# Optimization experiments

Measured on AMD Instinct MI355X. Metric: run time of the kernel, lower is better.

## Reference

```python
import jax, jax.numpy as jnp
import numpy as np

BETA = 0.9      # membrane decay
THRESH = 1.0    # firing threshold


def _lif(x):
    """Leaky integrate-and-fire over leading time axis. x: (T, ..., C) -> spikes (T, ..., C)."""
    def step(mem, xt):
        mem = BETA * mem + xt
        s = (mem > THRESH).astype(xt.dtype)
        mem = mem - s * THRESH  # soft reset
        return mem, s
    _, spikes = jax.lax.scan(step, jnp.zeros_like(x[0]), x)
    return spikes


def setup_inputs() -> dict:
    key = jax.random.key(0)
    k1, k2, k3, k4, k5 = jax.random.split(key, 5)
    T, N, D = 4, 8192, 1024
    E, EF, TOPK = 8, 512, 2  # expert_ff = d_ff // n_experts = 4096 // 8
    x = jax.random.normal(k1, (T, N, D), dtype=jnp.float32)
    expert_indices = jax.random.randint(k2, (N, TOPK), 0, E)
    expert_weights = jax.random.uniform(k3, (N, TOPK), dtype=jnp.float32)
    up_w = jax.random.normal(k4, (E, EF, D), dtype=jnp.float32) * 0.02   # Linear(d_model, ef).weight
    down_w = jax.random.normal(k5, (E, D, EF), dtype=jnp.float32) * 0.02  # Linear(ef, d_model).weight
    return {"x": x, "expert_indices": expert_indices, "expert_weights": expert_weights,
            "up_w": up_w, "down_w": down_w}


def reference(x, expert_indices, expert_weights, up_w, down_w):
    T, N, D = x.shape
    E = up_w.shape[0]
    # Dense combine weights W[n, e] = sum_k weights[n, k] * (indices[n, k] == e)
    W = jnp.zeros((N, E), dtype=x.dtype).at[
        jnp.arange(N)[:, None], expert_indices].add(expert_weights)
    out = jnp.zeros_like(x)
    for e in range(E):  # fixed small loop over experts
        h = _lif(jnp.einsum('tnd,fd->tnf', x, up_w[e]))   # up-proj + LIF hidden
        o = _lif(jnp.einsum('tnf,df->tnd', h, down_w[e]))  # down-proj + LIF output
        out = out + o * W[:, e][None, :, None]             # weighted combine (0 for inactive)
    return out
```

## Files before the change

kernel.cpp:

```cpp
#include <hip/hip_runtime.h>
#include <stdint.h>

#define T_STEPS 4
#define NTOK    8192
#define DMODEL  1024
#define NEXP    8
#define EFF     512
#define BMT     128
#define CAPTOT  (2*NTOK + NEXP*BMT)

typedef __attribute__((ext_vector_type(8))) short bf8_t;
typedef __attribute__((ext_vector_type(4))) float f32x4;

#define MFMA(a,b,c) __builtin_amdgcn_mfma_f32_16x16x32_bf16((a),(b),(c),0,0,0)


__device__ __forceinline__ unsigned short bf16rn(float f) {
    unsigned u = __float_as_uint(f);
    unsigned r = u + 0x7fffu + ((u >> 16) & 1u);
    return (unsigned short)(r >> 16);
}
__device__ __forceinline__ float bf2f(unsigned short h) {
    return __uint_as_float(((unsigned)h) << 16);
}
__device__ __forceinline__ unsigned pk(unsigned short a, unsigned short b) {
    return (unsigned)a | ((unsigned)b << 16);
}

__device__ __forceinline__ void stage8_3limb(const float* __restrict__ src,
                                             unsigned short* d0, unsigned short* d1,
                                             unsigned short* d2) {
    float v[8];
    *(float4*)&v[0] = *(const float4*)(src + 0);
    *(float4*)&v[4] = *(const float4*)(src + 4);
    unsigned short h[8], m[8], l[8];
#pragma unroll
    for (int i = 0; i < 8; ++i) {
        unsigned short a = bf16rn(v[i]);
        float r1 = v[i] - bf2f(a);
        unsigned short b = bf16rn(r1);
        float r2 = r1 - bf2f(b);
        h[i] = a; m[i] = b; l[i] = bf16rn(r2);
    }
    *(uint4*)d0 = make_uint4(pk(h[0],h[1]), pk(h[2],h[3]), pk(h[4],h[5]), pk(h[6],h[7]));
    *(uint4*)d1 = make_uint4(pk(m[0],m[1]), pk(m[2],m[3]), pk(m[4],m[5]), pk(m[6],m[7]));
    *(uint4*)d2 = make_uint4(pk(l[0],l[1]), pk(l[2],l[3]), pk(l[4],l[5]), pk(l[6],l[7]));
}


__global__ void k_split(const float* __restrict__ w, unsigned short* __restrict__ h,
                        unsigned short* __restrict__ m, unsigned short* __restrict__ l) {
    size_t i = (size_t)(blockIdx.x * blockDim.x + threadIdx.x) * 8;
    stage8_3limb(w + i, h + i, m + i, l + i);
}


__global__ void k_count(const int* __restrict__ idx, int* __restrict__ counts) {
    int n = blockIdx.x * blockDim.x + threadIdx.x;
    if (n >= NTOK) return;
    int e0 = idx[2*n], e1 = idx[2*n+1];
    atomicAdd(&counts[e0], 1);
    if (e1 != e0) atomicAdd(&counts[e1], 1);
}

__global__ void k_prefix(const int* __restrict__ counts, int* __restrict__ offsets) {
    if (threadIdx.x == 0) {
        int o = 0;
        for (int e = 0; e < NEXP; ++e) {
            offsets[e] = o;
            o += (counts[e] + BMT - 1) / BMT * BMT;
        }
        offsets[NEXP] = o;
    }
}

__global__ void k_fill(const int* __restrict__ idx, const float* __restrict__ wts,
                       const int* __restrict__ offsets, int* __restrict__ cursors,
                       int* __restrict__ tok, float* __restrict__ wgt) {
    int n = blockIdx.x * blockDim.x + threadIdx.x;
    if (n >= NTOK) return;
    int e0 = idx[2*n], e1 = idx[2*n+1];
    float w0 = wts[2*n], w1 = wts[2*n+1];
    if (e0 == e1) w0 = __fadd_rn(w0, w1);
    int p0 = offsets[e0] + atomicAdd(&cursors[e0], 1);
    tok[p0] = n; wgt[p0] = w0;
    if (e1 != e0) {
        int p1 = offsets[e1] + atomicAdd(&cursors[e1], 1);
        tok[p1] = n; wgt[p1] = w1;
    }
}


__global__ __launch_bounds__(256, 2)
void k_up(const float* __restrict__ x,
          const unsigned short* __restrict__ uwh, const unsigned short* __restrict__ uwm,
          const unsigned short* __restrict__ uwl,
          const int* __restrict__ offsets, const int* __restrict__ tok,
          unsigned short* __restrict__ spk) {
    const int m0 = blockIdx.x * BMT;
    const int ft = blockIdx.y;
    if (m0 >= offsets[NEXP]) return;
    int e = 0;
    for (int i = 1; i < NEXP; ++i) if (m0 >= offsets[i]) e = i;

    __shared__ unsigned short As[3][128][40];
    __shared__ unsigned short Bs[3][128][40];

    const int tid  = threadIdx.x;
    const int lane = tid & 63, wid = tid >> 6;
    const int quad = lane >> 4, l16 = lane & 15;
    const int mw = (wid & 1) * 64, nw = (wid >> 1) * 64;

    const int r = tid >> 1, half = tid & 1;
    const int tokA = tok[m0 + r];
    const float* xbase = x + (size_t)tokA * DMODEL + half * 16;
    const size_t woff = ((size_t)e * EFF + ft * 128 + r) * DMODEL + half * 16;
    const unsigned short* bhp = uwh + woff;
    const unsigned short* bmp = uwm + woff;
    const unsigned short* blp = uwl + woff;

    f32x4 mem[4][4];
#pragma unroll
    for (int i = 0; i < 4; ++i)
#pragma unroll
        for (int j = 0; j < 4; ++j) mem[i][j] = (f32x4){0.f,0.f,0.f,0.f};

    for (int t = 0; t < T_STEPS; ++t) {
        f32x4 acc[4][4];
#pragma unroll
        for (int i = 0; i < 4; ++i)
#pragma unroll
            for (int j = 0; j < 4; ++j) acc[i][j] = (f32x4){0.f,0.f,0.f,0.f};

        const float* xrow = xbase + (size_t)t * NTOK * DMODEL;

        for (int kc = 0; kc < DMODEL; kc += 32) {
            __syncthreads();
            stage8_3limb(xrow + kc,     &As[0][r][half*16],   &As[1][r][half*16],   &As[2][r][half*16]);
            stage8_3limb(xrow + kc + 8, &As[0][r][half*16+8], &As[1][r][half*16+8], &As[2][r][half*16+8]);
            *(uint4*)&Bs[0][r][half*16]   = *(const uint4*)(bhp + kc);
            *(uint4*)&Bs[0][r][half*16+8] = *(const uint4*)(bhp + kc + 8);
            *(uint4*)&Bs[1][r][half*16]   = *(const uint4*)(bmp + kc);
            *(uint4*)&Bs[1][r][half*16+8] = *(const uint4*)(bmp + kc + 8);
            *(uint4*)&Bs[2][r][half*16]   = *(const uint4*)(blp + kc);
            *(uint4*)&Bs[2][r][half*16+8] = *(const uint4*)(blp + kc + 8);
            __syncthreads();

            bf8_t bh[4], bm[4], bl[4];
#pragma unroll
            for (int nt = 0; nt < 4; ++nt) {
                const int nr = nw + nt*16 + l16;
                bh[nt] = *(const bf8_t*)&Bs[0][nr][quad*8];
                bm[nt] = *(const bf8_t*)&Bs[1][nr][quad*8];
                bl[nt] = *(const bf8_t*)&Bs[2][nr][quad*8];
            }
#pragma unroll
            for (int mt = 0; mt < 4; ++mt) {
                const int mr = mw + mt*16 + l16;
                bf8_t ah = *(const bf8_t*)&As[0][mr][quad*8];
                bf8_t am = *(const bf8_t*)&As[1][mr][quad*8];
                bf8_t al = *(const bf8_t*)&As[2][mr][quad*8];
#pragma unroll
                for (int nt = 0; nt < 4; ++nt) {
                    f32x4 c = acc[mt][nt];
                    c = MFMA(ah, bh[nt], c);
                    c = MFMA(am, bh[nt], c);
                    c = MFMA(ah, bm[nt], c);
                    c = MFMA(am, bm[nt], c);
                    c = MFMA(al, bh[nt], c);
                    c = MFMA(ah, bl[nt], c);
                    acc[mt][nt] = c;
                }
            }
        }

#pragma unroll
        for (int mt = 0; mt < 4; ++mt)
#pragma unroll
            for (int nt = 0; nt < 4; ++nt)
#pragma unroll
                for (int reg = 0; reg < 4; ++reg) {
                    float mv = __fadd_rn(__fmul_rn(0.9f, mem[mt][nt][reg]), acc[mt][nt][reg]);
                    bool s = mv > 1.0f;
                    mem[mt][nt][reg] = __fsub_rn(mv, s ? 1.0f : 0.0f);
                    int row = m0 + mw + mt*16 + quad*4 + reg;
                    int col = ft*128 + nw + nt*16 + l16;
                    spk[((size_t)t * CAPTOT + row) * EFF + col] = s ? 0x3F80u : 0u;
                }
    }
}


__global__ __launch_bounds__(256, 3)
void k_dn(const unsigned short* __restrict__ spk,
          const unsigned short* __restrict__ dwh, const unsigned short* __restrict__ dwm,
          const unsigned short* __restrict__ dwl,
          const int* __restrict__ offsets, const int* __restrict__ tok,
          const float* __restrict__ wgt, float* __restrict__ out) {
    const int m0 = blockIdx.x * BMT;
    const int dt = blockIdx.y;
    if (m0 >= offsets[NEXP]) return;
    int e = 0;
    for (int i = 1; i < NEXP; ++i) if (m0 >= offsets[i]) e = i;

    __shared__ unsigned short As[128][40];
    __shared__ unsigned short Bs[3][64][40];

    const int tid  = threadIdx.x;
    const int lane = tid & 63, wid = tid >> 6;
    const int quad = lane >> 4, l16 = lane & 15;
    const int mw = (wid & 1) * 64, nw = (wid >> 1) * 32;

    const int r = tid >> 1, half = tid & 1;
    const int dr = tid >> 2, q = tid & 3;
    const unsigned short* arow = spk + (size_t)(m0 + r) * EFF + half * 16;
    const size_t doff = ((size_t)e * DMODEL + dt * 64 + dr) * EFF + q * 8;
    const unsigned short* bhp = dwh + doff;
    const unsigned short* bmp = dwm + doff;
    const unsigned short* blp = dwl + doff;

    int   rn[4][4];
    float rw[4][4];
#pragma unroll
    for (int mt = 0; mt < 4; ++mt)
#pragma unroll
        for (int reg = 0; reg < 4; ++reg) {
            int rr = m0 + mw + mt*16 + quad*4 + reg;
            rn[mt][reg] = tok[rr];
            rw[mt][reg] = wgt[rr];
        }

    f32x4 mem[4][2];
#pragma unroll
    for (int i = 0; i < 4; ++i) { mem[i][0] = (f32x4){0.f,0.f,0.f,0.f}; mem[i][1] = (f32x4){0.f,0.f,0.f,0.f}; }

    for (int t = 0; t < T_STEPS; ++t) {
        f32x4 acc[4][2];
#pragma unroll
        for (int i = 0; i < 4; ++i) { acc[i][0] = (f32x4){0.f,0.f,0.f,0.f}; acc[i][1] = (f32x4){0.f,0.f,0.f,0.f}; }

        const unsigned short* at = arow + (size_t)t * CAPTOT * EFF;

        for (int kc = 0; kc < EFF; kc += 32) {
            __syncthreads();
            *(uint4*)&As[r][half*16 + 0] = *(const uint4*)(at + kc + 0);
            *(uint4*)&As[r][half*16 + 8] = *(const uint4*)(at + kc + 8);
            *(uint4*)&Bs[0][dr][q*8] = *(const uint4*)(bhp + kc);
            *(uint4*)&Bs[1][dr][q*8] = *(const uint4*)(bmp + kc);
            *(uint4*)&Bs[2][dr][q*8] = *(const uint4*)(blp + kc);
            __syncthreads();

            bf8_t bh[2], bm[2], bl[2];
#pragma unroll
            for (int nt = 0; nt < 2; ++nt) {
                const int nr = nw + nt*16 + l16;
                bh[nt] = *(const bf8_t*)&Bs[0][nr][quad*8];
                bm[nt] = *(const bf8_t*)&Bs[1][nr][quad*8];
                bl[nt] = *(const bf8_t*)&Bs[2][nr][quad*8];
            }
#pragma unroll
            for (int mt = 0; mt < 4; ++mt) {
                const int mr = mw + mt*16 + l16;
                bf8_t a = *(const bf8_t*)&As[mr][quad*8];
#pragma unroll
                for (int nt = 0; nt < 2; ++nt) {
                    f32x4 c = acc[mt][nt];
                    c = MFMA(a, bh[nt], c);
                    c = MFMA(a, bm[nt], c);
                    c = MFMA(a, bl[nt], c);
                    acc[mt][nt] = c;
                }
            }
        }

#pragma unroll
        for (int mt = 0; mt < 4; ++mt)
#pragma unroll
            for (int nt = 0; nt < 2; ++nt)
#pragma unroll
                for (int reg = 0; reg < 4; ++reg) {
                    float mv = __fadd_rn(__fmul_rn(0.9f, mem[mt][nt][reg]), acc[mt][nt][reg]);
                    bool s = mv > 1.0f;
                    mem[mt][nt][reg] = __fsub_rn(mv, s ? 1.0f : 0.0f);
                    float w = rw[mt][reg];
                    if (s && w != 0.0f) {
                        int col = dt*64 + nw + nt*16 + l16;
                        atomicAdd(out + ((size_t)t * NTOK + rn[mt][reg]) * DMODEL + col, w);
                    }
                }
    }
}


extern "C" void kernel_launch(void* const* d_in, const int* in_sizes, int n_in,
                              void* d_out, int out_size, void* d_ws, size_t ws_size,
                              hipStream_t stream) {
    const float* x      = (const float*)d_in[0];
    const int*   idx    = (const int*)  d_in[1];
    const float* wts    = (const float*)d_in[2];
    const float* up_w   = (const float*)d_in[3];
    const float* down_w = (const float*)d_in[4];
    float* out = (float*)d_out;

    char* ws = (char*)d_ws;
    int*   counts  = (int*)(ws + 0);
    int*   cursors = (int*)(ws + 32);
    int*   offsets = (int*)(ws + 64);
    int*   tok     = (int*)(ws + 128);
    float* wgt     = (float*)(ws + 128 + (size_t)CAPTOT * 4);
    unsigned short* spk = (unsigned short*)(ws + 128 + (size_t)CAPTOT * 8);

    const size_t WSPK = (size_t)T_STEPS * CAPTOT * EFF * 2;
    size_t base2 = 128 + (size_t)CAPTOT * 8 + WSPK;
    base2 = (base2 + 511) & ~(size_t)511;
    const size_t WLIMB = (size_t)NEXP * EFF * DMODEL * 2;
    unsigned short* uwh = (unsigned short*)(ws + base2);
    unsigned short* uwm = (unsigned short*)(ws + base2 + 1*WLIMB);
    unsigned short* uwl = (unsigned short*)(ws + base2 + 2*WLIMB);
    unsigned short* dwh = (unsigned short*)(ws + base2 + 3*WLIMB);
    unsigned short* dwm = (unsigned short*)(ws + base2 + 4*WLIMB);
    unsigned short* dwl = (unsigned short*)(ws + base2 + 5*WLIMB);

    hipMemsetAsync(ws, 0, 128 + (size_t)CAPTOT * 8, stream);
    hipMemsetAsync(out, 0, (size_t)out_size * sizeof(float), stream);

    const int nsplit = NEXP * EFF * DMODEL / 8 / 256;
    k_split<<<nsplit, 256, 0, stream>>>(up_w,   uwh, uwm, uwl);
    k_split<<<nsplit, 256, 0, stream>>>(down_w, dwh, dwm, dwl);

    k_count <<<(NTOK + 255) / 256, 256, 0, stream>>>(idx, counts);
    k_prefix<<<1, 64, 0, stream>>>(counts, offsets);
    k_fill  <<<(NTOK + 255) / 256, 256, 0, stream>>>(idx, wts, offsets, cursors, tok, wgt);

    dim3 gup(CAPTOT / BMT, EFF / 128);
    k_up<<<gup, 256, 0, stream>>>(x, uwh, uwm, uwl, offsets, tok, spk);

    dim3 gdn(CAPTOT / BMT, DMODEL / 64);
    k_dn<<<gdn, 256, 0, stream>>>(spk, dwh, dwm, dwl, offsets, tok, wgt, out);
}
```

Baseline: 1.071 ms.

## Swizzle LDS tiles, widen down-proj tile to 128 columns, raise k_up occupancy

Replaces the padded LDS rows (stride 40) with unpadded 32-wide rows that use an XOR column swizzle, which shrinks shared memory and is meant to avoid bank conflicts. k_up's launch bound rises to 3 blocks per CU, since the smaller LDS footprint allows it. k_dn now computes a 128x128 output tile per block instead of 128x64, halving the grid in the D dimension and the number of times each spike tile is reloaded. Token and weight lookups move into the epilogue to save registers. The larger accumulator set in k_dn raises register pressure and may reduce its occupancy.

```diff
diff --git a/kernel.cpp b/kernel.cpp
--- a/kernel.cpp
+++ b/kernel.cpp
@@ -13,6 +13,8 @@
 typedef __attribute__((ext_vector_type(4))) float f32x4;
 
 #define MFMA(a,b,c) __builtin_amdgcn_mfma_f32_16x16x32_bf16((a),(b),(c),0,0,0)
+
+#define SWZC(r, c) ((((c) ^ (((r) >> 1) & 3))) * 8)
 
 
 __device__ __forceinline__ unsigned short bf16rn(float f) {
@@ -91,7 +93,7 @@
 }
 
 
-__global__ __launch_bounds__(256, 2)
+__global__ __launch_bounds__(256, 3)
 void k_up(const float* __restrict__ x,
           const unsigned short* __restrict__ uwh, const unsigned short* __restrict__ uwm,
           const unsigned short* __restrict__ uwl,
@@ -103,8 +105,8 @@
     int e = 0;
     for (int i = 1; i < NEXP; ++i) if (m0 >= offsets[i]) e = i;
 
-    __shared__ unsigned short As[3][128][40];
-    __shared__ unsigned short Bs[3][128][40];
+    __shared__ unsigned short As[3][128][32];
+    __shared__ unsigned short Bs[3][128][32];
 
     const int tid  = threadIdx.x;
     const int lane = tid & 63, wid = tid >> 6;
@@ -112,6 +114,8 @@
     const int mw = (wid & 1) * 64, nw = (wid >> 1) * 64;
 
     const int r = tid >> 1, half = tid & 1;
+    const int c0 = SWZC(r, half*2 + 0);
+    const int c1 = SWZC(r, half*2 + 1);
     const int tokA = tok[m0 + r];
     const float* xbase = x + (size_t)tokA * DMODEL + half * 16;
     const size_t woff = ((size_t)e * EFF + ft * 128 + r) * DMODEL + half * 16;
@@ -119,6 +123,8 @@
     const unsigned short* bmp = uwm + woff;
     const unsigned short* blp = uwl + woff;
 
+    const int kq = SWZC(l16, quad);
+
     f32x4 mem[4][4];
 #pragma unroll
     for (int i = 0; i < 4; ++i)
@@ -136,30 +142,30 @@
 
         for (int kc = 0; kc < DMODEL; kc += 32) {
             __syncthreads();
-            stage8_3limb(xrow + kc,     &As[0][r][half*16],   &As[1][r][half*16],   &As[2][r][half*16]);
-            stage8_3limb(xrow + kc + 8, &As[0][r][half*16+8], &As[1][r][half*16+8], &As[2][r][half*16+8]);
-            *(uint4*)&Bs[0][r][half*16]   = *(const uint4*)(bhp + kc);
-            *(uint4*)&Bs[0][r][half*16+8] = *(const uint4*)(bhp + kc + 8);
-            *(uint4*)&Bs[1][r][half*16]   = *(const uint4*)(bmp + kc);
-            *(uint4*)&Bs[1][r][half*16+8] = *(const uint4*)(bmp + kc + 8);
-            *(uint4*)&Bs[2][r][half*16]   = *(const uint4*)(blp + kc);
-            *(uint4*)&Bs[2][r][half*16+8] = *(const uint4*)(blp + kc + 8);
+            stage8_3limb(xrow + kc,     &As[0][r][c0], &As[1][r][c0], &As[2][r][c0]);
+            stage8_3limb(xrow + kc + 8, &As[0][r][c1], &As[1][r][c1], &As[2][r][c1]);
+            *(uint4*)&Bs[0][r][c0] = *(const uint4*)(bhp + kc);
+            *(uint4*)&Bs[0][r][c1] = *(const uint4*)(bhp + kc + 8);
+            *(uint4*)&Bs[1][r][c0] = *(const uint4*)(bmp + kc);
+            *(uint4*)&Bs[1][r][c1] = *(const uint4*)(bmp + kc + 8);
+            *(uint4*)&Bs[2][r][c0] = *(const uint4*)(blp + kc);
+            *(uint4*)&Bs[2][r][c1] = *(const uint4*)(blp + kc + 8);
             __syncthreads();
 
             bf8_t bh[4], bm[4], bl[4];
 #pragma unroll
             for (int nt = 0; nt < 4; ++nt) {
                 const int nr = nw + nt*16 + l16;
-                bh[nt] = *(const bf8_t*)&Bs[0][nr][quad*8];
-                bm[nt] = *(const bf8_t*)&Bs[1][nr][quad*8];
-                bl[nt] = *(const bf8_t*)&Bs[2][nr][quad*8];
+                bh[nt] = *(const bf8_t*)&Bs[0][nr][kq];
+                bm[nt] = *(const bf8_t*)&Bs[1][nr][kq];
+                bl[nt] = *(const bf8_t*)&Bs[2][nr][kq];
             }
 #pragma unroll
             for (int mt = 0; mt < 4; ++mt) {
                 const int mr = mw + mt*16 + l16;
-                bf8_t ah = *(const bf8_t*)&As[0][mr][quad*8];
-                bf8_t am = *(const bf8_t*)&As[1][mr][quad*8];
-                bf8_t al = *(const bf8_t*)&As[2][mr][quad*8];
+                bf8_t ah = *(const bf8_t*)&As[0][mr][kq];
+                bf8_t am = *(const bf8_t*)&As[1][mr][kq];
+                bf8_t al = *(const bf8_t*)&As[2][mr][kq];
 #pragma unroll
                 for (int nt = 0; nt < 4; ++nt) {
                     f32x4 c = acc[mt][nt];
@@ -203,67 +209,66 @@
     int e = 0;
     for (int i = 1; i < NEXP; ++i) if (m0 >= offsets[i]) e = i;
 
-    __shared__ unsigned short As[128][40];
-    __shared__ unsigned short Bs[3][64][40];
+    __shared__ unsigned short As[128][32];
+    __shared__ unsigned short Bs[3][128][32];
 
     const int tid  = threadIdx.x;
     const int lane = tid & 63, wid = tid >> 6;
     const int quad = lane >> 4, l16 = lane & 15;
-    const int mw = (wid & 1) * 64, nw = (wid >> 1) * 32;
+    const int mw = (wid & 1) * 64, nw = (wid >> 1) * 64;
 
     const int r = tid >> 1, half = tid & 1;
-    const int dr = tid >> 2, q = tid & 3;
+    const int c0 = SWZC(r, half*2 + 0);
+    const int c1 = SWZC(r, half*2 + 1);
     const unsigned short* arow = spk + (size_t)(m0 + r) * EFF + half * 16;
-    const size_t doff = ((size_t)e * DMODEL + dt * 64 + dr) * EFF + q * 8;
+    const size_t doff = ((size_t)e * DMODEL + dt * 128 + r) * EFF + half * 16;
     const unsigned short* bhp = dwh + doff;
     const unsigned short* bmp = dwm + doff;
     const unsigned short* blp = dwl + doff;
 
-    int   rn[4][4];
-    float rw[4][4];
-#pragma unroll
-    for (int mt = 0; mt < 4; ++mt)
-#pragma unroll
-        for (int reg = 0; reg < 4; ++reg) {
-            int rr = m0 + mw + mt*16 + quad*4 + reg;
-            rn[mt][reg] = tok[rr];
-            rw[mt][reg] = wgt[rr];
-        }
-
-    f32x4 mem[4][2];
-#pragma unroll
-    for (int i = 0; i < 4; ++i) { mem[i][0] = (f32x4){0.f,0.f,0.f,0.f}; mem[i][1] = (f32x4){0.f,0.f,0.f,0.f}; }
+    const int kq = SWZC(l16, quad);
+
+    f32x4 mem[4][4];
+#pragma unroll
+    for (int i = 0; i < 4; ++i)
+#pragma unroll
+        for (int j = 0; j < 4; ++j) mem[i][j] = (f32x4){0.f,0.f,0.f,0.f};
 
     for (int t = 0; t < T_STEPS; ++t) {
-        f32x4 acc[4][2];
-#pragma unroll
-        for (int i = 0; i < 4; ++i) { acc[i][0] = (f32x4){0.f,0.f,0.f,0.f}; acc[i][1] = (f32x4){0.f,0.f,0.f,0.f}; }
+        f32x4 acc[4][4];
+#pragma unroll
+        for (int i = 0; i < 4; ++i)
+#pragma unroll
+            for (int j = 0; j < 4; ++j) acc[i][j] = (f32x4){0.f,0.f,0.f,0.f};
 
         const unsigned short* at = arow + (size_t)t * CAPTOT * EFF;
 
         for (int kc = 0; kc < EFF; kc += 32) {
             __syncthreads();
-            *(uint4*)&As[r][half*16 + 0] = *(const uint4*)(at + kc + 0);
-            *(uint4*)&As[r][half*16 + 8] = *(const uint4*)(at + kc + 8);
-            *(uint4*)&Bs[0][dr][q*8] = *(const uint4*)(bhp + kc);
-            *(uint4*)&Bs[1][dr][q*8] = *(const uint4*)(bmp + kc);
-            *(uint4*)&Bs[2][dr][q*8] = *(const uint4*)(blp + kc);
+            *(uint4*)&As[r][c0] = *(const uint4*)(at + kc + 0);
+            *(uint4*)&As[r][c1] = *(const uint4*)(at + kc + 8);
+            *(uint4*)&Bs[0][r][c0] = *(const uint4*)(bhp + kc);
+            *(uint4*)&Bs[0][r][c1] = *(const uint4*)(bhp + kc + 8);
+            *(uint4*)&Bs[1][r][c0] = *(const uint4*)(bmp + kc);
+            *(uint4*)&Bs[1][r][c1] = *(const uint4*)(bmp + kc + 8);
+            *(uint4*)&Bs[2][r][c0] = *(const uint4*)(blp + kc);
+            *(uint4*)&Bs[2][r][c1] = *(const uint4*)(blp + kc + 8);
             __syncthreads();
 
-            bf8_t bh[2], bm[2], bl[2];
-#pragma unroll
-            for (int nt = 0; nt < 2; ++nt) {
+            bf8_t bh[4], bm[4], bl[4];
+#pragma unroll
+            for (int nt = 0; nt < 4; ++nt) {
                 const int nr = nw + nt*16 + l16;
-                bh[nt] = *(const bf8_t*)&Bs[0][nr][quad*8];
-                bm[nt] = *(const bf8_t*)&Bs[1][nr][quad*8];
-                bl[nt] = *(const bf8_t*)&Bs[2][nr][quad*8];
+                bh[nt] = *(const bf8_t*)&Bs[0][nr][kq];
+                bm[nt] = *(const bf8_t*)&Bs[1][nr][kq];
+                bl[nt] = *(const bf8_t*)&Bs[2][nr][kq];
             }
 #pragma unroll
             for (int mt = 0; mt < 4; ++mt) {
                 const int mr = mw + mt*16 + l16;
-                bf8_t a = *(const bf8_t*)&As[mr][quad*8];
-#pragma unroll
-                for (int nt = 0; nt < 2; ++nt) {
+                bf8_t a = *(const bf8_t*)&As[mr][kq];
+#pragma unroll
+                for (int nt = 0; nt < 4; ++nt) {
                     f32x4 c = acc[mt][nt];
                     c = MFMA(a, bh[nt], c);
                     c = MFMA(a, bm[nt], c);
@@ -274,20 +279,24 @@
         }
 
 #pragma unroll
-        for (int mt = 0; mt < 4; ++mt)
-#pragma unroll
-            for (int nt = 0; nt < 2; ++nt)
-#pragma unroll
-                for (int reg = 0; reg < 4; ++reg) {
+        for (int mt = 0; mt < 4; ++mt) {
+            const int rbase = m0 + mw + mt*16 + quad*4;
+#pragma unroll
+            for (int reg = 0; reg < 4; ++reg) {
+                const int   n = tok[rbase + reg];
+                const float w = wgt[rbase + reg];
+#pragma unroll
+                for (int nt = 0; nt < 4; ++nt) {
                     float mv = __fadd_rn(__fmul_rn(0.9f, mem[mt][nt][reg]), acc[mt][nt][reg]);
                     bool s = mv > 1.0f;
                     mem[mt][nt][reg] = __fsub_rn(mv, s ? 1.0f : 0.0f);
-                    float w = rw[mt][reg];
                     if (s && w != 0.0f) {
-                        int col = dt*64 + nw + nt*16 + l16;
-                        atomicAdd(out + ((size_t)t * NTOK + rn[mt][reg]) * DMODEL + col, w);
+                        int col = dt*128 + nw + nt*16 + l16;
+                        atomicAdd(out + ((size_t)t * NTOK + n) * DMODEL + col, w);
                     }
                 }
+            }
+        }
     }
 }
 
@@ -335,6 +344,6 @@
     dim3 gup(CAPTOT / BMT, EFF / 128);
     k_up<<<gup, 256, 0, stream>>>(x, uwh, uwm, uwl, offsets, tok, spk);
 
-    dim3 gdn(CAPTOT / BMT, DMODEL / 64);
+    dim3 gdn(CAPTOT / BMT, DMODEL / 128);
     k_dn<<<gdn, 256, 0, stream>>>(spk, dwh, dwm, dwl, offsets, tok, wgt, out);
 }
```

New measurement: 1.370 ms. +27.9%, slower.
